# Kernel tuning notes

Measured on AMD Instinct MI355X. Metric: run time of the kernel, lower is better.

## Reference

```python
import jax, jax.numpy as jnp
import numpy as np

D_IN = 1024
D_OUT = 1024
N_HEADS = 16
HEAD_DIM = D_IN // N_HEADS


def setup_inputs() -> dict:
    key = jax.random.key(0)
    k0, k1, k2, k3, k4, k5 = jax.random.split(key, 6)
    s = 1.0 / np.sqrt(D_IN)
    return {
        "input_embeddings": jax.random.normal(k0, (4, 2048, D_IN), dtype=jnp.float32),
        "Wq": jax.random.normal(k1, (D_IN, D_IN), dtype=jnp.float32) * s,
        "Wk": jax.random.normal(k2, (D_IN, D_IN), dtype=jnp.float32) * s,
        "Wv": jax.random.normal(k3, (D_IN, D_IN), dtype=jnp.float32) * s,
        "Wo": jax.random.normal(k4, (D_IN, D_OUT), dtype=jnp.float32) * s,
        "bo": jax.random.normal(k5, (D_OUT,), dtype=jnp.float32) * 0.01,
    }


def reference(input_embeddings, Wq, Wk, Wv, Wo, bo):
    B, T, D = input_embeddings.shape
    x = input_embeddings
    # QKV projections (no bias), split into heads: (B, H, T, hd)
    def split(y):
        return y.reshape(B, T, N_HEADS, HEAD_DIM).transpose(0, 2, 1, 3)
    Q = split(x @ Wq)
    K = split(x @ Wk)
    V = split(x @ Wv)
    scale = 1.0 / np.sqrt(HEAD_DIM)
    scores = jnp.einsum("bhqd,bhkd->bhqk", Q, K) * scale  # (B,H,T,T)
    causal = jnp.tril(jnp.ones((T, T), dtype=bool))
    scores = jnp.where(causal, scores, -jnp.inf)
    probs = jax.nn.softmax(scores, axis=-1)  # dropout p=0 -> identity
    out = jnp.einsum("bhqk,bhkd->bhqd", probs, V)
    out = out.transpose(0, 2, 1, 3).reshape(B, T, D)
    return out @ Wo + bo
```

## Files before the change

### kernel.cpp

```cpp
#include <hip/hip_runtime.h>
#include <hip/hip_bf16.h>
#include <math.h>

typedef __attribute__((ext_vector_type(8))) short short8;
typedef __attribute__((ext_vector_type(4))) float f32x4;

#define MFMA_BF16 __builtin_amdgcn_mfma_f32_16x16x32_bf16

static constexpr int Dm = 1024;
static constexpr int Tm = 2048;
static constexpr int Bb = 4;
static constexpr int NHm = 16;
static constexpr int HDm = 64;
static constexpr int Mtot = Bb * Tm;
static constexpr int NKT = Tm / 64;
static constexpr float kQScale = 0.125f * 1.4426950408889634f;

__device__ __forceinline__ unsigned short f2bf(float f) {
  unsigned int u = __float_as_uint(f);
  u += 0x7FFFu + ((u >> 16) & 1u);
  return (unsigned short)(u >> 16);
}

__device__ __forceinline__ float fexp2(float x) {
  float r;
  asm("v_exp_f32 %0, %1" : "=v"(r) : "v"(x));
  return r;
}

__device__ __forceinline__ void gload16(const void* g, void* l) {
  __builtin_amdgcn_global_load_lds((const __attribute__((address_space(1))) void*)g,
                                   (__attribute__((address_space(3))) void*)l, 16, 0, 0);
}

__global__ __launch_bounds__(256) void cvt_kernel(const float* __restrict__ src,
                                                  short* __restrict__ dst, int n) {
  int stride = gridDim.x * blockDim.x;
  for (int i = blockIdx.x * blockDim.x + threadIdx.x; i * 4 < n; i += stride) {
    float4 v = reinterpret_cast<const float4*>(src)[i];
    short4 o;
    o.x = (short)f2bf(v.x);
    o.y = (short)f2bf(v.y);
    o.z = (short)f2bf(v.z);
    o.w = (short)f2bf(v.w);
    reinterpret_cast<short4*>(dst)[i] = o;
  }
}

__global__ __launch_bounds__(256) void cvt_t_kernel(
    const float* __restrict__ W0, const float* __restrict__ W1,
    const float* __restrict__ W2, const float* __restrict__ W3,
    short* __restrict__ T0, short* __restrict__ T1,
    short* __restrict__ T2, short* __restrict__ T3) {
  const float* W = blockIdx.z == 0 ? W0 : blockIdx.z == 1 ? W1 : blockIdx.z == 2 ? W2 : W3;
  short* Wt = blockIdx.z == 0 ? T0 : blockIdx.z == 1 ? T1 : blockIdx.z == 2 ? T2 : T3;
  __shared__ __align__(16) short T[64 * 72];
  const int tid = threadIdx.x;
  const int k0 = blockIdx.y * 64, n0 = blockIdx.x * 64;
#pragma unroll
  for (int p = 0; p < 4; ++p) {
    int idx = tid + p * 256;
    int kr = idx >> 4, c4 = (idx & 15) * 4;
    float4 v = *reinterpret_cast<const float4*>(W + (size_t)(k0 + kr) * Dm + n0 + c4);
    T[(c4 + 0) * 72 + kr] = (short)f2bf(v.x);
    T[(c4 + 1) * 72 + kr] = (short)f2bf(v.y);
    T[(c4 + 2) * 72 + kr] = (short)f2bf(v.z);
    T[(c4 + 3) * 72 + kr] = (short)f2bf(v.w);
  }
  __syncthreads();
#pragma unroll
  for (int p = 0; p < 2; ++p) {
    int idx = tid + p * 256;
    int nr = idx >> 3, c8 = (idx & 7) * 8;
    *reinterpret_cast<short8*>(Wt + (size_t)(n0 + nr) * Dm + k0 + c8) =
        *reinterpret_cast<const short8*>(&T[nr * 72 + c8]);
  }
}

template <int MODE>
__global__ __launch_bounds__(256) void gemm_bt_kernel(
    const short* __restrict__ Ags, const short* __restrict__ Bts,
    short* __restrict__ Cbf, float* __restrict__ Cf, const float* __restrict__ bias) {
  __shared__ __align__(16) short As[128 * 32];
  __shared__ __align__(16) short Bs[128 * 32];
  const int tid = threadIdx.x;
  const int lane = tid & 63;
  const int w = tid >> 6;
  const int wr = (w >> 1) * 64, wc = (w & 1) * 64;
  const int g = lane >> 4;
  const int lr = lane & 15;
  const int m0 = blockIdx.y * 128;
  const int n0 = blockIdx.x * 128;
  const int rowt = tid >> 2;
  const int cg8 = (tid & 3) * 8;

  f32x4 acc[4][4];
#pragma unroll
  for (int mi = 0; mi < 4; ++mi)
#pragma unroll
    for (int ni = 0; ni < 4; ++ni)
#pragma unroll
      for (int r = 0; r < 4; ++r) acc[mi][ni][r] = 0.f;

  for (int kt = 0; kt < Dm / 32; ++kt) {
    __syncthreads();
#pragma unroll
    for (int p = 0; p < 2; ++p) {
      gload16(Ags + (size_t)(m0 + p * 64 + rowt) * Dm + kt * 32 + cg8,
              &As[(p * 64 + w * 16) * 32]);
      gload16(Bts + (size_t)(n0 + p * 64 + rowt) * Dm + kt * 32 + cg8,
              &Bs[(p * 64 + w * 16) * 32]);
    }
    __syncthreads();
    short8 a[4], b[4];
#pragma unroll
    for (int mi = 0; mi < 4; ++mi)
      a[mi] = *reinterpret_cast<const short8*>(&As[(wr + mi * 16 + lr) * 32 + g * 8]);
#pragma unroll
    for (int ni = 0; ni < 4; ++ni)
      b[ni] = *reinterpret_cast<const short8*>(&Bs[(wc + ni * 16 + lr) * 32 + g * 8]);
#pragma unroll
    for (int mi = 0; mi < 4; ++mi)
#pragma unroll
      for (int ni = 0; ni < 4; ++ni)
        acc[mi][ni] = MFMA_BF16(a[mi], b[ni], acc[mi][ni], 0, 0, 0);
  }

#pragma unroll
  for (int mi = 0; mi < 4; ++mi)
#pragma unroll
    for (int ni = 0; ni < 4; ++ni)
#pragma unroll
      for (int r = 0; r < 4; ++r) {
        int mg = m0 + wr + mi * 16 + g * 4 + r;
        int ng = n0 + wc + ni * 16 + lr;
        float v = acc[mi][ni][r];
        int b_ = mg >> 11, t_ = mg & 2047, h_ = ng >> 6, d_ = ng & 63;
        size_t bh = (size_t)(b_ * NHm + h_);
        if (MODE == 0) {
          Cbf[(bh * Tm + t_) * HDm + d_] = (short)f2bf(v * kQScale);
        } else if (MODE == 1) {
          Cbf[((bh * NKT + (t_ >> 6)) << 12) + (t_ & 63) * 64 + (d_ ^ ((t_ & 7) << 3))] =
              (short)f2bf(v);
        } else if (MODE == 2) {
          Cbf[((bh * NKT + (t_ >> 6)) << 12) + d_ * 64 + ((t_ & 63) ^ ((d_ & 7) << 3))] =
              (short)f2bf(v);
        } else {
          Cf[(size_t)mg * Dm + ng] = v + bias[ng];
        }
      }
}

__global__ __launch_bounds__(256) void attn_kernel(
    const short* __restrict__ Qg, const short* __restrict__ Kg,
    const short* __restrict__ Vg, short* __restrict__ Og) {
  __shared__ __align__(16) short Kl[2][64 * 64];
  __shared__ __align__(16) short Vl[2][64 * 64];
  __shared__ __align__(16) short Pl[4][32 * 72];
  const int tid = threadIdx.x;
  const int lane = tid & 63;
  const int w = tid >> 6;
  const int g = lane >> 4;
  const int lr = lane & 15;
  const int bh = blockIdx.y;
  const int pi = blockIdx.x;
  const short* Ks = Kg + ((size_t)bh * NKT << 12);
  const short* Vs = Vg + ((size_t)bh * NKT << 12);
  short* Pw = &Pl[w][0];
  const int b_ = bh >> 4, h_ = bh & 15;

  short8 ones;
#pragma unroll
  for (int j = 0; j < 8; ++j) ones[j] = (short)0x3F80;

  auto stage = [&](int t, int buf) {
#pragma unroll
    for (int i = 0; i < 2; ++i) {
      int ch = w * 2 + i;
      gload16(Ks + ((size_t)t << 12) + ch * 512 + lane * 8, &Kl[buf][ch * 512]);
      gload16(Vs + ((size_t)t << 12) + ch * 512 + lane * 8, &Vl[buf][ch * 512]);
    }
  };

  for (int pass = 0; pass < 2; ++pass) {
    const int qb = pass == 0 ? (15 - pi) : pi;
    const int q0 = qb * 128;
    const int qw = q0 + w * 32;
    const short* Qs = Qg + ((size_t)bh * Tm + q0) * HDm;

    short8 qf[2][2];
#pragma unroll
    for (int mi = 0; mi < 2; ++mi)
#pragma unroll
      for (int kk = 0; kk < 2; ++kk)
        qf[mi][kk] = *reinterpret_cast<const short8*>(
            Qs + (w * 32 + mi * 16 + lr) * HDm + kk * 32 + g * 8);

    f32x4 o[2][4], lacc[2];
#pragma unroll
    for (int mi = 0; mi < 2; ++mi)
#pragma unroll
      for (int r = 0; r < 4; ++r) {
        lacc[mi][r] = 0.f;
#pragma unroll
        for (int di = 0; di < 4; ++di) o[mi][di][r] = 0.f;
      }

    const int nt = q0 / 64 + 2;
    stage(0, 0);
    __syncthreads();
    int cur = 0;
    for (int t = 0; t < nt; ++t) {
      if (t + 1 < nt) stage(t + 1, cur ^ 1);
      const int k0 = t * 64;
      const bool active = (k0 <= qw + 31);
      if (active) {
        short8 kf[2][4];
#pragma unroll
        for (int ni = 0; ni < 4; ++ni) {
          int row = ni * 16 + lr;
#pragma unroll
          for (int kk = 0; kk < 2; ++kk)
            kf[kk][ni] = *reinterpret_cast<const short8*>(
                &Kl[cur][row * 64 + ((kk * 32 + g * 8) ^ ((row & 7) << 3))]);
        }
        f32x4 s[2][4];
#pragma unroll
        for (int mi = 0; mi < 2; ++mi)
#pragma unroll
          for (int ni = 0; ni < 4; ++ni) {
            f32x4 acc;
#pragma unroll
            for (int r = 0; r < 4; ++r) acc[r] = 0.f;
            acc = MFMA_BF16(qf[mi][0], kf[0][ni], acc, 0, 0, 0);
            acc = MFMA_BF16(qf[mi][1], kf[1][ni], acc, 0, 0, 0);
            s[mi][ni] = acc;
          }
        if (k0 + 63 > qw) {
#pragma unroll
          for (int mi = 0; mi < 2; ++mi)
#pragma unroll
            for (int ni = 0; ni < 4; ++ni)
#pragma unroll
              for (int r = 0; r < 4; ++r)
                if (k0 + ni * 16 + lr > qw + mi * 16 + g * 4 + r) s[mi][ni][r] = -1e30f;
        }
#pragma unroll
        for (int mi = 0; mi < 2; ++mi)
#pragma unroll
          for (int ni = 0; ni < 4; ++ni)
#pragma unroll
            for (int r = 0; r < 4; ++r)
              Pw[(mi * 16 + g * 4 + r) * 72 + ((ni * 16 + lr) ^ (g << 4))] =
                  (short)f2bf(fexp2(s[mi][ni][r]));

#pragma unroll
        for (int kk = 0; kk < 2; ++kk) {
          short8 pf[2];
#pragma unroll
          for (int mi = 0; mi < 2; ++mi)
            pf[mi] = *reinterpret_cast<const short8*>(
                &Pw[(mi * 16 + lr) * 72 + ((kk * 32 + g * 8) ^ ((lr >> 2) << 4))]);
#pragma unroll
          for (int mi = 0; mi < 2; ++mi)
            lacc[mi] = MFMA_BF16(pf[mi], ones, lacc[mi], 0, 0, 0);
#pragma unroll
          for (int di = 0; di < 4; ++di) {
            int d = di * 16 + lr;
            short8 vf = *reinterpret_cast<const short8*>(
                &Vl[cur][d * 64 + ((kk * 32 + g * 8) ^ ((d & 7) << 3))]);
#pragma unroll
            for (int mi = 0; mi < 2; ++mi)
              o[mi][di] = MFMA_BF16(pf[mi], vf, o[mi][di], 0, 0, 0);
          }
        }
      }
      __syncthreads();
      cur ^= 1;
    }

#pragma unroll
    for (int mi = 0; mi < 2; ++mi)
#pragma unroll
      for (int di = 0; di < 4; ++di)
#pragma unroll
        for (int r = 0; r < 4; ++r) {
          float ov = o[mi][di][r] / lacc[mi][r];
          int qg = q0 + w * 32 + mi * 16 + g * 4 + r;
          int d_ = di * 16 + lr;
          Og[((size_t)b_ * Tm + qg) * Dm + h_ * HDm + d_] = (short)f2bf(ov);
        }
  }
}

extern "C" void kernel_launch(void* const* d_in, const int* in_sizes, int n_in,
                              void* d_out, int out_size, void* d_ws, size_t ws_size,
                              hipStream_t stream) {
  const float* X = (const float*)d_in[0];
  const float* Wq = (const float*)d_in[1];
  const float* Wk = (const float*)d_in[2];
  const float* Wv = (const float*)d_in[3];
  const float* Wo = (const float*)d_in[4];
  const float* bo = (const float*)d_in[5];
  float* out = (float*)d_out;

  char* ws = (char*)d_ws;
  short* Xb = (short*)ws;  ws += (size_t)Mtot * Dm * 2;
  short* Wqt = (short*)ws; ws += (size_t)Dm * Dm * 2;
  short* Wkt = (short*)ws; ws += (size_t)Dm * Dm * 2;
  short* Wvt = (short*)ws; ws += (size_t)Dm * Dm * 2;
  short* Wot = (short*)ws; ws += (size_t)Dm * Dm * 2;
  short* Qb = (short*)ws;  ws += (size_t)Mtot * Dm * 2;
  short* Kb = (short*)ws;  ws += (size_t)Mtot * Dm * 2;
  short* Vb = (short*)ws;  ws += (size_t)Mtot * Dm * 2;
  short* Ab = (short*)ws;  ws += (size_t)Mtot * Dm * 2;

  cvt_kernel<<<dim3(1024), dim3(256), 0, stream>>>(X, Xb, Mtot * Dm);
  cvt_t_kernel<<<dim3(16, 16, 4), dim3(256), 0, stream>>>(Wq, Wk, Wv, Wo, Wqt, Wkt, Wvt, Wot);

  dim3 ggrid(Dm / 128, Mtot / 128);
  gemm_bt_kernel<0><<<ggrid, 256, 0, stream>>>(Xb, Wqt, Qb, nullptr, nullptr);
  gemm_bt_kernel<1><<<ggrid, 256, 0, stream>>>(Xb, Wkt, Kb, nullptr, nullptr);
  gemm_bt_kernel<2><<<ggrid, 256, 0, stream>>>(Xb, Wvt, Vb, nullptr, nullptr);

  attn_kernel<<<dim3(8, Bb * NHm), 256, 0, stream>>>(Qb, Kb, Vb, Ab);

  gemm_bt_kernel<3><<<ggrid, 256, 0, stream>>>(Ab, Wot, nullptr, out, bo);
}
```

Baseline: 211.9 us.

## Merge QKV GEMMs into one launch and triple-buffer attention K/V loads

Replaces the three separate Q/K/V projection launches with a single launch that uses blockIdx.z to pick the weight and output layout, cutting launch gaps and filling the GPU with one larger grid. The attention kernel moves from double to triple buffering of K/V tiles, with an explicit vmcnt wait and a single barrier per iteration, so loads run two tiles ahead. The attention grid is also transposed so consecutive blocks cover different heads rather than different query chunks. In exchange it uses more shared memory per attention block, which may lower occupancy, and relies on hand-counted vmcnt values for correctness.

```diff
diff --git a/kernel.cpp b/kernel.cpp
--- a/kernel.cpp
+++ b/kernel.cpp
@@ -77,10 +77,84 @@
   }
 }
 
-template <int MODE>
-__global__ __launch_bounds__(256) void gemm_bt_kernel(
+__global__ __launch_bounds__(256) void gemm_qkv_kernel(
+    const short* __restrict__ Ags, const short* __restrict__ Wq,
+    const short* __restrict__ Wk, const short* __restrict__ Wv,
+    short* __restrict__ Qo, short* __restrict__ Ko, short* __restrict__ Vo) {
+  __shared__ __align__(16) short As[128 * 32];
+  __shared__ __align__(16) short Bs[128 * 32];
+  const int z = blockIdx.z;
+  const short* Bts = z == 0 ? Wq : z == 1 ? Wk : Wv;
+  short* Co = z == 0 ? Qo : z == 1 ? Ko : Vo;
+  const int tid = threadIdx.x;
+  const int lane = tid & 63;
+  const int w = tid >> 6;
+  const int wr = (w >> 1) * 64, wc = (w & 1) * 64;
+  const int g = lane >> 4;
+  const int lr = lane & 15;
+  const int m0 = blockIdx.y * 128;
+  const int n0 = blockIdx.x * 128;
+  const int rowt = tid >> 2;
+  const int cg8 = (tid & 3) * 8;
+
+  f32x4 acc[4][4];
+#pragma unroll
+  for (int mi = 0; mi < 4; ++mi)
+#pragma unroll
+    for (int ni = 0; ni < 4; ++ni)
+#pragma unroll
+      for (int r = 0; r < 4; ++r) acc[mi][ni][r] = 0.f;
+
+  for (int kt = 0; kt < Dm / 32; ++kt) {
+    __syncthreads();
+#pragma unroll
+    for (int p = 0; p < 2; ++p) {
+      gload16(Ags + (size_t)(m0 + p * 64 + rowt) * Dm + kt * 32 + cg8,
+              &As[(p * 64 + w * 16) * 32]);
+      gload16(Bts + (size_t)(n0 + p * 64 + rowt) * Dm + kt * 32 + cg8,
+              &Bs[(p * 64 + w * 16) * 32]);
+    }
+    __syncthreads();
+    short8 a[4], b[4];
+#pragma unroll
+    for (int mi = 0; mi < 4; ++mi)
+      a[mi] = *reinterpret_cast<const short8*>(&As[(wr + mi * 16 + lr) * 32 + g * 8]);
+#pragma unroll
+    for (int ni = 0; ni < 4; ++ni)
+      b[ni] = *reinterpret_cast<const short8*>(&Bs[(wc + ni * 16 + lr) * 32 + g * 8]);
+#pragma unroll
+    for (int mi = 0; mi < 4; ++mi)
+#pragma unroll
+      for (int ni = 0; ni < 4; ++ni)
+        acc[mi][ni] = MFMA_BF16(a[mi], b[ni], acc[mi][ni], 0, 0, 0);
+  }
+
+#pragma unroll
+  for (int mi = 0; mi < 4; ++mi)
+#pragma unroll
+    for (int ni = 0; ni < 4; ++ni)
+#pragma unroll
+      for (int r = 0; r < 4; ++r) {
+        int mg = m0 + wr + mi * 16 + g * 4 + r;
+        int ng = n0 + wc + ni * 16 + lr;
+        float v = acc[mi][ni][r];
+        int b_ = mg >> 11, t_ = mg & 2047, h_ = ng >> 6, d_ = ng & 63;
+        size_t bh = (size_t)(b_ * NHm + h_);
+        if (z == 0) {
+          Co[(bh * Tm + t_) * HDm + d_] = (short)f2bf(v * kQScale);
+        } else if (z == 1) {
+          Co[((bh * NKT + (t_ >> 6)) << 12) + (t_ & 63) * 64 + (d_ ^ ((t_ & 7) << 3))] =
+              (short)f2bf(v);
+        } else {
+          Co[((bh * NKT + (t_ >> 6)) << 12) + d_ * 64 + ((t_ & 63) ^ ((d_ & 7) << 3))] =
+              (short)f2bf(v);
+        }
+      }
+}
+
+__global__ __launch_bounds__(256) void gemm_out_kernel(
     const short* __restrict__ Ags, const short* __restrict__ Bts,
-    short* __restrict__ Cbf, float* __restrict__ Cf, const float* __restrict__ bias) {
+    float* __restrict__ Cf, const float* __restrict__ bias) {
   __shared__ __align__(16) short As[128 * 32];
   __shared__ __align__(16) short Bs[128 * 32];
   const int tid = threadIdx.x;
@@ -134,36 +208,23 @@
       for (int r = 0; r < 4; ++r) {
         int mg = m0 + wr + mi * 16 + g * 4 + r;
         int ng = n0 + wc + ni * 16 + lr;
-        float v = acc[mi][ni][r];
-        int b_ = mg >> 11, t_ = mg & 2047, h_ = ng >> 6, d_ = ng & 63;
-        size_t bh = (size_t)(b_ * NHm + h_);
-        if (MODE == 0) {
-          Cbf[(bh * Tm + t_) * HDm + d_] = (short)f2bf(v * kQScale);
-        } else if (MODE == 1) {
-          Cbf[((bh * NKT + (t_ >> 6)) << 12) + (t_ & 63) * 64 + (d_ ^ ((t_ & 7) << 3))] =
-              (short)f2bf(v);
-        } else if (MODE == 2) {
-          Cbf[((bh * NKT + (t_ >> 6)) << 12) + d_ * 64 + ((t_ & 63) ^ ((d_ & 7) << 3))] =
-              (short)f2bf(v);
-        } else {
-          Cf[(size_t)mg * Dm + ng] = v + bias[ng];
-        }
+        Cf[(size_t)mg * Dm + ng] = acc[mi][ni][r] + bias[ng];
       }
 }
 
 __global__ __launch_bounds__(256) void attn_kernel(
     const short* __restrict__ Qg, const short* __restrict__ Kg,
     const short* __restrict__ Vg, short* __restrict__ Og) {
-  __shared__ __align__(16) short Kl[2][64 * 64];
-  __shared__ __align__(16) short Vl[2][64 * 64];
+  __shared__ __align__(16) short Kl[3][64 * 64];
+  __shared__ __align__(16) short Vl[3][64 * 64];
   __shared__ __align__(16) short Pl[4][32 * 72];
   const int tid = threadIdx.x;
   const int lane = tid & 63;
   const int w = tid >> 6;
   const int g = lane >> 4;
   const int lr = lane & 15;
-  const int bh = blockIdx.y;
-  const int pi = blockIdx.x;
+  const int bh = blockIdx.x;
+  const int pi = blockIdx.y;
   const short* Ks = Kg + ((size_t)bh * NKT << 12);
   const short* Vs = Vg + ((size_t)bh * NKT << 12);
   short* Pw = &Pl[w][0];
@@ -208,10 +269,14 @@
 
     const int nt = q0 / 64 + 2;
     stage(0, 0);
-    __syncthreads();
-    int cur = 0;
+    stage(1, 1);
     for (int t = 0; t < nt; ++t) {
-      if (t + 1 < nt) stage(t + 1, cur ^ 1);
+      if (t < nt - 1) asm volatile("s_waitcnt vmcnt(4)" ::: "memory");
+      else            asm volatile("s_waitcnt vmcnt(0)" ::: "memory");
+      __builtin_amdgcn_s_barrier();
+      __builtin_amdgcn_sched_barrier(0);
+      if (t + 2 < nt) stage(t + 2, (t + 2) % 3);
+      const int cur = t % 3;
       const int k0 = t * 64;
       const bool active = (k0 <= qw + 31);
       if (active) {
@@ -275,9 +340,8 @@
           }
         }
       }
-      __syncthreads();
-      cur ^= 1;
     }
+    __syncthreads();
 
 #pragma unroll
     for (int mi = 0; mi < 2; ++mi)
@@ -318,12 +382,10 @@
   cvt_kernel<<<dim3(1024), dim3(256), 0, stream>>>(X, Xb, Mtot * Dm);
   cvt_t_kernel<<<dim3(16, 16, 4), dim3(256), 0, stream>>>(Wq, Wk, Wv, Wo, Wqt, Wkt, Wvt, Wot);
 
-  dim3 ggrid(Dm / 128, Mtot / 128);
-  gemm_bt_kernel<0><<<ggrid, 256, 0, stream>>>(Xb, Wqt, Qb, nullptr, nullptr);
-  gemm_bt_kernel<1><<<ggrid, 256, 0, stream>>>(Xb, Wkt, Kb, nullptr, nullptr);
-  gemm_bt_kernel<2><<<ggrid, 256, 0, stream>>>(Xb, Wvt, Vb, nullptr, nullptr);
-
-  attn_kernel<<<dim3(8, Bb * NHm), 256, 0, stream>>>(Qb, Kb, Vb, Ab);
-
-  gemm_bt_kernel<3><<<ggrid, 256, 0, stream>>>(Ab, Wot, nullptr, out, bo);
-}
+  gemm_qkv_kernel<<<dim3(Dm / 128, Mtot / 128, 3), 256, 0, stream>>>(
+      Xb, Wqt, Wkt, Wvt, Qb, Kb, Vb);
+
+  attn_kernel<<<dim3(Bb * NHm, 8), 256, 0, stream>>>(Qb, Kb, Vb, Ab);
+
+  gemm_out_kernel<<<dim3(Dm / 128, Mtot / 128), 256, 0, stream>>>(Ab, Wot, out, bo);
+}
```

Result: faster. 195.1 us (-7.9%).

## Fuse QKV GEMMs into a 256x256 ping-pong MFMA kernel and triple-buffer attention

Applied to the files above, without the earlier changes.

Replaces the 128x128 single-buffered GEMM with a 512-thread kernel that computes a 256x256 tile. It uses a 64-wide K step, XOR-swizzled LDS double buffering and an eight-phase schedule that interleaves global-to-LDS loads with MFMA quads under explicit barriers and priority hints. The three Q/K/V projections become one launch by treating the consecutively allocated Wq/Wk/Wv transposes as a single 3072-row operand, and the output epilogue picks the destination by column block. Attention moves to three LDS buffers with a prefetch distance of two and vmcnt-based waits, and swaps grid axes. The larger tiles cut redundant global traffic and launches, but the output GEMM has only 128 blocks and the large LDS footprint leaves one block per CU.

```diff
diff --git a/kernel.cpp b/kernel.cpp
--- a/kernel.cpp
+++ b/kernel.cpp
@@ -14,6 +14,7 @@
 static constexpr int HDm = 64;
 static constexpr int Mtot = Bb * Tm;
 static constexpr int NKT = Tm / 64;
+static constexpr int NTILE = Dm / 64;
 static constexpr float kQScale = 0.125f * 1.4426950408889634f;
 
 __device__ __forceinline__ unsigned short f2bf(float f) {
@@ -77,76 +78,159 @@
   }
 }
 
+
+#define READA(CUR, MH)                                                        \
+  {                                                                           \
+    _Pragma("unroll") for (int mf = 0; mf < 4; ++mf) {                        \
+      const int row_ = wr * 128 + (MH) * 64 + mf * 16 + lr;                   \
+      _Pragma("unroll") for (int kk = 0; kk < 2; ++kk)                        \
+          af[mf][kk] = *reinterpret_cast<const short8*>(                      \
+              &AsL[CUR][row_ * 64 + (((kk * 4 + g) ^ (lr & 7)) << 3)]);       \
+    }                                                                         \
+  }
+
+#define READB(CUR, NH)                                                        \
+  {                                                                           \
+    _Pragma("unroll") for (int nf = 0; nf < 2; ++nf) {                        \
+      const int row_ = wc * 64 + (NH) * 32 + nf * 16 + lr;                    \
+      _Pragma("unroll") for (int kk = 0; kk < 2; ++kk)                        \
+          bf[nf][kk] = *reinterpret_cast<const short8*>(                      \
+              &BsL[CUR][row_ * 64 + (((kk * 4 + g) ^ (lr & 7)) << 3)]);       \
+    }                                                                         \
+  }
+
+#define QUAD(MH, NH)                                                          \
+  {                                                                           \
+    __builtin_amdgcn_s_setprio(1);                                            \
+    _Pragma("unroll") for (int mf = 0; mf < 4; ++mf) {                        \
+      _Pragma("unroll") for (int nf = 0; nf < 2; ++nf) {                      \
+        acc[(MH) * 4 + mf][(NH) * 2 + nf] = MFMA_BF16(                        \
+            af[mf][0], bf[nf][0], acc[(MH) * 4 + mf][(NH) * 2 + nf], 0, 0, 0);\
+        acc[(MH) * 4 + mf][(NH) * 2 + nf] = MFMA_BF16(                        \
+            af[mf][1], bf[nf][1], acc[(MH) * 4 + mf][(NH) * 2 + nf], 0, 0, 0);\
+      }                                                                       \
+    }                                                                         \
+    __builtin_amdgcn_s_setprio(0);                                            \
+  }
+
+#define PHASE_TAIL                                                            \
+  asm volatile("s_waitcnt lgkmcnt(0)" ::: "memory");                          \
+  __builtin_amdgcn_s_barrier();                                               \
+  __builtin_amdgcn_sched_barrier(0);
+
+#define PHASE_TAIL_VM(COND)                                                   \
+  asm volatile("s_waitcnt lgkmcnt(0)" ::: "memory");                          \
+  if (COND) asm volatile("s_waitcnt vmcnt(4)" ::: "memory");                  \
+  else      asm volatile("s_waitcnt vmcnt(0)" ::: "memory");                  \
+  __builtin_amdgcn_s_barrier();                                               \
+  __builtin_amdgcn_sched_barrier(0);
+
+#define PHASE_MID                                                             \
+  __builtin_amdgcn_s_barrier();                                               \
+  __builtin_amdgcn_sched_barrier(0);
+
 template <int MODE>
-__global__ __launch_bounds__(256) void gemm_bt_kernel(
+__global__ __launch_bounds__(512, 1) void gemm8_kernel(
     const short* __restrict__ Ags, const short* __restrict__ Bts,
-    short* __restrict__ Cbf, float* __restrict__ Cf, const float* __restrict__ bias) {
-  __shared__ __align__(16) short As[128 * 32];
-  __shared__ __align__(16) short Bs[128 * 32];
+    short* __restrict__ Qo, short* __restrict__ Ko, short* __restrict__ Vo,
+    float* __restrict__ Cf, const float* __restrict__ bias) {
+  __shared__ __align__(16) short AsL[2][256 * 64];
+  __shared__ __align__(16) short BsL[2][256 * 64];
   const int tid = threadIdx.x;
   const int lane = tid & 63;
   const int w = tid >> 6;
-  const int wr = (w >> 1) * 64, wc = (w & 1) * 64;
+  const int wr = w >> 2;
+  const int wc = w & 3;
   const int g = lane >> 4;
   const int lr = lane & 15;
-  const int m0 = blockIdx.y * 128;
-  const int n0 = blockIdx.x * 128;
-  const int rowt = tid >> 2;
-  const int cg8 = (tid & 3) * 8;
-
-  f32x4 acc[4][4];
-#pragma unroll
-  for (int mi = 0; mi < 4; ++mi)
+  const int m0 = blockIdx.x * 256;
+  const int n0g = blockIdx.y * 256;
+  const int sr8 = w * 8 + (lane >> 3);
+  const int sch = ((lane & 7) ^ (lane >> 3)) << 3;
+
+  auto stageH = [&](const short* G, int grow0, int kt, short* Ld) {
+#pragma unroll
+    for (int j = 0; j < 2; ++j)
+      gload16(G + (size_t)(grow0 + j * 64 + sr8) * Dm + kt * 64 + sch,
+              Ld + (j * 64 + w * 8) * 64);
+  };
+
+  f32x4 acc[8][4];
+#pragma unroll
+  for (int mi = 0; mi < 8; ++mi)
 #pragma unroll
     for (int ni = 0; ni < 4; ++ni)
 #pragma unroll
       for (int r = 0; r < 4; ++r) acc[mi][ni][r] = 0.f;
 
-  for (int kt = 0; kt < Dm / 32; ++kt) {
-    __syncthreads();
-#pragma unroll
-    for (int p = 0; p < 2; ++p) {
-      gload16(Ags + (size_t)(m0 + p * 64 + rowt) * Dm + kt * 32 + cg8,
-              &As[(p * 64 + w * 16) * 32]);
-      gload16(Bts + (size_t)(n0 + p * 64 + rowt) * Dm + kt * 32 + cg8,
-              &Bs[(p * 64 + w * 16) * 32]);
-    }
-    __syncthreads();
-    short8 a[4], b[4];
-#pragma unroll
-    for (int mi = 0; mi < 4; ++mi)
-      a[mi] = *reinterpret_cast<const short8*>(&As[(wr + mi * 16 + lr) * 32 + g * 8]);
+  short8 af[4][2], bf[2][2];
+
+  stageH(Ags, m0, 0, &AsL[0][0]);
+  stageH(Bts, n0g, 0, &BsL[0][0]);
+  stageH(Ags, m0 + 128, 0, &AsL[0][128 * 64]);
+  stageH(Bts, n0g + 128, 0, &BsL[0][128 * 64]);
+  stageH(Ags, m0, 1, &AsL[1][0]);
+  stageH(Bts, n0g, 1, &BsL[1][0]);
+  asm volatile("s_waitcnt vmcnt(4)" ::: "memory");
+  __builtin_amdgcn_s_barrier();
+  __builtin_amdgcn_sched_barrier(0);
+
+  for (int i = 0; i < NTILE / 2; ++i) {
+    const int t0 = 2 * i, t1 = 2 * i + 1;
+    const bool s0 = (t0 + 2 < NTILE), s1 = (t1 + 2 < NTILE);
+    READA(0, 0); READB(0, 0);
+    stageH(Ags, m0 + 128, t1, &AsL[1][128 * 64]);
+    PHASE_MID; QUAD(0, 0); PHASE_TAIL;
+    READB(0, 1);
+    stageH(Bts, n0g + 128, t1, &BsL[1][128 * 64]);
+    PHASE_MID; QUAD(0, 1); PHASE_TAIL;
+    READA(0, 1); READB(0, 0);
+    if (s0) stageH(Ags, m0, t0 + 2, &AsL[0][0]);
+    PHASE_MID; QUAD(1, 0); PHASE_TAIL;
+    READB(0, 1);
+    if (s0) stageH(Bts, n0g, t0 + 2, &BsL[0][0]);
+    PHASE_MID; QUAD(1, 1); PHASE_TAIL_VM(s0);
+    READA(1, 0); READB(1, 0);
+    if (s0) stageH(Ags, m0 + 128, t0 + 2, &AsL[0][128 * 64]);
+    PHASE_MID; QUAD(0, 0); PHASE_TAIL;
+    READB(1, 1);
+    if (s0) stageH(Bts, n0g + 128, t0 + 2, &BsL[0][128 * 64]);
+    PHASE_MID; QUAD(0, 1); PHASE_TAIL;
+    READA(1, 1); READB(1, 0);
+    if (s1) stageH(Ags, m0, t1 + 2, &AsL[1][0]);
+    PHASE_MID; QUAD(1, 0); PHASE_TAIL;
+    READB(1, 1);
+    if (s1) stageH(Bts, n0g, t1 + 2, &BsL[1][0]);
+    PHASE_MID; QUAD(1, 1); PHASE_TAIL_VM(s1);
+  }
+
+  const int z = n0g >> 10;
+  const int n0 = n0g & 1023;
+  short* Co = (MODE == 0) ? (z == 0 ? Qo : z == 1 ? Ko : Vo) : nullptr;
+#pragma unroll
+  for (int mi = 0; mi < 8; ++mi)
 #pragma unroll
     for (int ni = 0; ni < 4; ++ni)
-      b[ni] = *reinterpret_cast<const short8*>(&Bs[(wc + ni * 16 + lr) * 32 + g * 8]);
-#pragma unroll
-    for (int mi = 0; mi < 4; ++mi)
-#pragma unroll
-      for (int ni = 0; ni < 4; ++ni)
-        acc[mi][ni] = MFMA_BF16(a[mi], b[ni], acc[mi][ni], 0, 0, 0);
-  }
-
-#pragma unroll
-  for (int mi = 0; mi < 4; ++mi)
-#pragma unroll
-    for (int ni = 0; ni < 4; ++ni)
 #pragma unroll
       for (int r = 0; r < 4; ++r) {
-        int mg = m0 + wr + mi * 16 + g * 4 + r;
-        int ng = n0 + wc + ni * 16 + lr;
+        int mg = m0 + wr * 128 + mi * 16 + g * 4 + r;
         float v = acc[mi][ni][r];
-        int b_ = mg >> 11, t_ = mg & 2047, h_ = ng >> 6, d_ = ng & 63;
-        size_t bh = (size_t)(b_ * NHm + h_);
-        if (MODE == 0) {
-          Cbf[(bh * Tm + t_) * HDm + d_] = (short)f2bf(v * kQScale);
-        } else if (MODE == 1) {
-          Cbf[((bh * NKT + (t_ >> 6)) << 12) + (t_ & 63) * 64 + (d_ ^ ((t_ & 7) << 3))] =
-              (short)f2bf(v);
-        } else if (MODE == 2) {
-          Cbf[((bh * NKT + (t_ >> 6)) << 12) + d_ * 64 + ((t_ & 63) ^ ((d_ & 7) << 3))] =
-              (short)f2bf(v);
+        if (MODE == 1) {
+          int ng = n0g + wc * 64 + ni * 16 + lr;
+          Cf[(size_t)mg * Dm + ng] = v + bias[ng];
         } else {
-          Cf[(size_t)mg * Dm + ng] = v + bias[ng];
+          int ng = n0 + wc * 64 + ni * 16 + lr;
+          int b_ = mg >> 11, t_ = mg & 2047, h_ = ng >> 6, d_ = ng & 63;
+          size_t bh = (size_t)(b_ * NHm + h_);
+          if (z == 0) {
+            Co[(bh * Tm + t_) * HDm + d_] = (short)f2bf(v * kQScale);
+          } else if (z == 1) {
+            Co[((bh * NKT + (t_ >> 6)) << 12) + (t_ & 63) * 64 + (d_ ^ ((t_ & 7) << 3))] =
+                (short)f2bf(v);
+          } else {
+            Co[((bh * NKT + (t_ >> 6)) << 12) + d_ * 64 + ((t_ & 63) ^ ((d_ & 7) << 3))] =
+                (short)f2bf(v);
+          }
         }
       }
 }
@@ -154,16 +238,16 @@
 __global__ __launch_bounds__(256) void attn_kernel(
     const short* __restrict__ Qg, const short* __restrict__ Kg,
     const short* __restrict__ Vg, short* __restrict__ Og) {
-  __shared__ __align__(16) short Kl[2][64 * 64];
-  __shared__ __align__(16) short Vl[2][64 * 64];
+  __shared__ __align__(16) short Kl[3][64 * 64];
+  __shared__ __align__(16) short Vl[3][64 * 64];
   __shared__ __align__(16) short Pl[4][32 * 72];
   const int tid = threadIdx.x;
   const int lane = tid & 63;
   const int w = tid >> 6;
   const int g = lane >> 4;
   const int lr = lane & 15;
-  const int bh = blockIdx.y;
-  const int pi = blockIdx.x;
+  const int bh = blockIdx.x;
+  const int pi = blockIdx.y;
   const short* Ks = Kg + ((size_t)bh * NKT << 12);
   const short* Vs = Vg + ((size_t)bh * NKT << 12);
   short* Pw = &Pl[w][0];
@@ -208,10 +292,14 @@
 
     const int nt = q0 / 64 + 2;
     stage(0, 0);
-    __syncthreads();
-    int cur = 0;
+    stage(1, 1);
     for (int t = 0; t < nt; ++t) {
-      if (t + 1 < nt) stage(t + 1, cur ^ 1);
+      if (t < nt - 1) asm volatile("s_waitcnt vmcnt(4)" ::: "memory");
+      else            asm volatile("s_waitcnt vmcnt(0)" ::: "memory");
+      __builtin_amdgcn_s_barrier();
+      __builtin_amdgcn_sched_barrier(0);
+      if (t + 2 < nt) stage(t + 2, (t + 2) % 3);
+      const int cur = t % 3;
       const int k0 = t * 64;
       const bool active = (k0 <= qw + 31);
       if (active) {
@@ -275,9 +363,8 @@
           }
         }
       }
-      __syncthreads();
-      cur ^= 1;
     }
+    __syncthreads();
 
 #pragma unroll
     for (int mi = 0; mi < 2; ++mi)
@@ -318,12 +405,11 @@
   cvt_kernel<<<dim3(1024), dim3(256), 0, stream>>>(X, Xb, Mtot * Dm);
   cvt_t_kernel<<<dim3(16, 16, 4), dim3(256), 0, stream>>>(Wq, Wk, Wv, Wo, Wqt, Wkt, Wvt, Wot);
 
-  dim3 ggrid(Dm / 128, Mtot / 128);
-  gemm_bt_kernel<0><<<ggrid, 256, 0, stream>>>(Xb, Wqt, Qb, nullptr, nullptr);
-  gemm_bt_kernel<1><<<ggrid, 256, 0, stream>>>(Xb, Wkt, Kb, nullptr, nullptr);
-  gemm_bt_kernel<2><<<ggrid, 256, 0, stream>>>(Xb, Wvt, Vb, nullptr, nullptr);
-
-  attn_kernel<<<dim3(8, Bb * NHm), 256, 0, stream>>>(Qb, Kb, Vb, Ab);
-
-  gemm_bt_kernel<3><<<ggrid, 256, 0, stream>>>(Ab, Wot, nullptr, out, bo);
-}
+  gemm8_kernel<0><<<dim3(Mtot / 256, 3 * Dm / 256), 512, 0, stream>>>(
+      Xb, Wqt, Qb, Kb, Vb, nullptr, nullptr);
+
+  attn_kernel<<<dim3(Bb * NHm, 8), 256, 0, stream>>>(Qb, Kb, Vb, Ab);
+
+  gemm8_kernel<1><<<dim3(Mtot / 256, Dm / 256), 512, 0, stream>>>(
+      Ab, Wot, nullptr, nullptr, nullptr, out, bo);
+}
```

New measurement: 203.1 us. 1.04x faster.
